# Kernel optimization log

Hardware: AMD Instinct MI355X
Metric: run time of the kernel (lower is better)

## Reference

```python
import jax, jax.numpy as jnp
import numpy as np

B, C, H, W = 8, 64, 56, 56
PLANES = 64
EPS = 1e-5


def conv2d(x, w, b, stride=1, pad=1):
    out = jax.lax.conv_general_dilated(
        x, w, window_strides=(stride, stride), padding=[(pad, pad), (pad, pad)],
        dimension_numbers=('NCHW', 'OIHW', 'NCHW'))
    return out + b[None, :, None, None]


def _bilinear_gather(img, py, px):
    # img: [C,H,W]; py/px: [K2,Ho,Wo] float sample coords; zero outside bounds
    Ci, Hi, Wi = img.shape
    y0 = jnp.floor(py); x0 = jnp.floor(px)
    wy1 = py - y0; wx1 = px - x0
    wy0 = 1.0 - wy1; wx0 = 1.0 - wx1

    def g(yc, xc):
        valid = ((yc >= 0) & (yc < Hi) & (xc >= 0) & (xc < Wi)).astype(img.dtype)
        yi = jnp.clip(yc, 0, Hi - 1).astype(jnp.int32)
        xi = jnp.clip(xc, 0, Wi - 1).astype(jnp.int32)
        return img[:, yi, xi] * valid[None]  # [C,K2,Ho,Wo]

    return (g(y0, x0) * (wy0 * wx0)[None] + g(y0, x0 + 1) * (wy0 * wx1)[None]
            + g(y0 + 1, x0) * (wy1 * wx0)[None] + g(y0 + 1, x0 + 1) * (wy1 * wx1)[None])


def deform_conv2d(x, offset, weight, stride, pad, dil):
    # torchvision DeformConv2d semantics (no mask). offset: [B, 2*K2, Ho, Wo]
    Bx, Cx, Hx, Wx = x.shape
    O, _, kh, kw = weight.shape
    K2 = kh * kw
    Ho, Wo = offset.shape[2], offset.shape[3]
    off = offset.reshape(Bx, K2, 2, Ho, Wo)
    dy, dx = off[:, :, 0], off[:, :, 1]
    ki, kj = jnp.meshgrid(jnp.arange(kh), jnp.arange(kw), indexing='ij')
    base_y = (ki.reshape(-1) * dil - pad).astype(x.dtype)  # [K2]
    base_x = (kj.reshape(-1) * dil - pad).astype(x.dtype)
    hg = (jnp.arange(Ho) * stride).astype(x.dtype)
    wg = (jnp.arange(Wo) * stride).astype(x.dtype)
    py = dy + base_y[None, :, None, None] + hg[None, None, :, None]
    px = dx + base_x[None, :, None, None] + wg[None, None, None, :]
    cols = jax.vmap(_bilinear_gather)(x, py, px)  # [B,C,K2,Ho,Wo]
    return jnp.einsum('bckhw,ock->bohw', cols, weight.reshape(O, Cx, K2))


def bn(x, gamma, beta, mean, var):
    inv = gamma / jnp.sqrt(var + EPS)
    return x * inv[None, :, None, None] + (beta - mean * inv)[None, :, None, None]


def setup_inputs() -> dict:
    key = jax.random.key(0)
    ks = jax.random.split(key, 12)
    s = 0.05
    d = {
        'x':   jax.random.normal(ks[0], (B, C, H, W), jnp.float32),
        'ow1': jax.random.normal(ks[1], (2 * 9, C, 3, 3), jnp.float32) * s,
        'ob1': jnp.zeros((2 * 9,), jnp.float32),
        'ow3': jax.random.normal(ks[2], (2 * 25, C, 3, 3), jnp.float32) * s,
        'ob3': jnp.zeros((2 * 25,), jnp.float32),
        'ow2': jax.random.normal(ks[3], (2 * 9, PLANES, 3, 3), jnp.float32) * s,
        'ob2': jnp.zeros((2 * 9,), jnp.float32),
        'w1':  jax.random.normal(ks[4], (PLANES, C, 3, 3), jnp.float32) * s,
        'w3':  jax.random.normal(ks[5], (PLANES, C, 5, 5), jnp.float32) * s,
        'w2':  jax.random.normal(ks[6], (PLANES, PLANES, 3, 3), jnp.float32) * s,
    }
    for i, tag in zip((7, 8, 9), ('1', '3', '2')):
        d['g' + tag] = jnp.ones((PLANES,), jnp.float32)
        d['b' + tag] = jnp.zeros((PLANES,), jnp.float32)
        d['m' + tag] = jax.random.normal(ks[i], (PLANES,), jnp.float32) * 0.1
        d['v' + tag] = jnp.ones((PLANES,), jnp.float32)
    return d


def reference(x, ow1, ob1, ow3, ob3, ow2, ob2, w1, w3, w2,
              g1, b1, m1, v1, g3, b3, m3, v3, g2, b2, m2, v2):
    offset1 = conv2d(x, ow1, ob1, stride=1, pad=1)
    out = jax.nn.relu(bn(deform_conv2d(x, offset1, w1, 1, 2, 2), g1, b1, m1, v1))
    offset3 = conv2d(x, ow3, ob3, stride=1, pad=1)
    out_1 = jax.nn.relu(bn(deform_conv2d(x, offset3, w3, 1, 4, 2), g3, b3, m3, v3))
    out = out + out_1
    offset2 = conv2d(out, ow2, ob2, stride=1, pad=1)
    out = bn(deform_conv2d(out, offset2, w2, 1, 2, 2), g2, b2, m2, v2)
    out = out + x  # identity shortcut (stride=1, in_planes==planes)
    return jax.nn.relu(out)
```

## Files before the change

kernel.cpp:

```cpp
#include <hip/hip_runtime.h>
#include <math.h>

#define HD 56
#define WD 56
#define CD 64
#define PLANE 3136

typedef _Float16 f16x8 __attribute__((ext_vector_type(8)));
typedef _Float16 f16x4 __attribute__((ext_vector_type(4)));
typedef _Float16 f16x2 __attribute__((ext_vector_type(2)));
typedef float    f32x4 __attribute__((ext_vector_type(4)));

__global__ __launch_bounds__(256) void wtrans_k(
    const float* __restrict__ w1, const float* __restrict__ w3, const float* __restrict__ w2,
    const float* __restrict__ ow1, const float* __restrict__ ow3, const float* __restrict__ ow2,
    _Float16* __restrict__ t1, _Float16* __restrict__ t3, _Float16* __restrict__ t2,
    _Float16* __restrict__ owF, _Float16* __restrict__ owT2)
{
    int y = blockIdx.y;
    if (y == 0 || y == 1 || y == 2) {
        const float* src = (y == 0) ? w1 : (y == 1) ? w3 : w2;
        _Float16* dst    = (y == 0) ? t1 : (y == 1) ? t3 : t2;
        int K2 = (y == 1) ? 25 : 9;
        int total = 64 * 64 * K2;
        for (int idx = blockIdx.x * 256 + threadIdx.x; idx < total; idx += gridDim.x * 256) {
            int k = idx >> 12;
            int o = (idx >> 6) & 63;
            int c = idx & 63;
            dst[idx] = (_Float16)src[(o * 64 + c) * K2 + k];
        }
    } else if (y == 3) {
        int total = 9 * 32 * 64;
        for (int idx = blockIdx.x * 256 + threadIdx.x; idx < total; idx += gridDim.x * 256) {
            int k = idx >> 11;
            int o = (idx >> 6) & 31;
            int c = idx & 63;
            owF[k * 6144 + o * 64 + c] = (o < 18) ? (_Float16)ow1[(o * 64 + c) * 9 + k] : (_Float16)0.f;
        }
    } else if (y == 4) {
        int total = 9 * 64 * 64;
        for (int idx = blockIdx.x * 256 + threadIdx.x; idx < total; idx += gridDim.x * 256) {
            int k = idx >> 12;
            int o = (idx >> 6) & 63;
            int c = idx & 63;
            owF[k * 6144 + (32 + o) * 64 + c] = (o < 50) ? (_Float16)ow3[(o * 64 + c) * 9 + k] : (_Float16)0.f;
        }
    } else {
        int total = 9 * 32 * 64;
        for (int idx = blockIdx.x * 256 + threadIdx.x; idx < total; idx += gridDim.x * 256) {
            int k = idx >> 11;
            int o = (idx >> 6) & 31;
            int c = idx & 63;
            owT2[k * 2048 + o * 64 + c] = (o < 18) ? (_Float16)ow2[(o * 64 + c) * 9 + k] : (_Float16)0.f;
        }
    }
}

__global__ __launch_bounds__(256) void xt_k(const float* __restrict__ src, _Float16* __restrict__ dst)
{
    int b  = blockIdx.y;
    int px = blockIdx.x * 64 + (threadIdx.x & 63);
    int cg = threadIdx.x >> 6;
    const float* s = src + (size_t)b * CD * PLANE + px;
    f16x8 lo, hi;
#pragma unroll
    for (int i = 0; i < 8; ++i) lo[i] = (_Float16)s[(cg * 16 + i) * PLANE];
#pragma unroll
    for (int i = 0; i < 8; ++i) hi[i] = (_Float16)s[(cg * 16 + 8 + i) * PLANE];
    _Float16* d = dst + ((size_t)b * PLANE + px) * 64 + cg * 16;
    *(f16x8*)d = lo;
    *(f16x8*)(d + 8) = hi;
}

template<int NTILES, int OP>
__device__ inline void af_load(const _Float16* __restrict__ ow, int k, int off, f16x8* s) {
    const _Float16* wk = ow + k * (OP * 64);
#pragma unroll
    for (int t = 0; t < NTILES; ++t) s[t] = *(const f16x8*)(wk + (t * 16) * 64 + off);
}

template<int FUSED>
__global__ __launch_bounds__(256) void offc_k(
    const _Float16* __restrict__ src,
    const _Float16* __restrict__ ow,
    const float* __restrict__ biasA, const float* __restrict__ biasB,
    uint4* __restrict__ tbl)
{
    constexpr int NTILES = FUSED ? 6 : 2;
    constexpr int OP     = FUSED ? 96 : 32;
    constexpr int NTT    = FUSED ? 34 : 9;
    __shared__ float red[4][NTILES * 4 * 64];

    int tid = threadIdx.x;
    int bid = blockIdx.x;
    int b    = bid & 7;
    int tile = bid >> 3;
    int l = tid & 63;
    int n = l & 15;
    int g = l >> 4;
    int w = tid >> 6;
    int tg = w >> 1;
    int pix = tile * 16 + n;
    int ho = pix / WD, wo = pix - ho * WD;
    int ckoff = (w & 1) * 32 + g * 8;
    int afo = n * 64 + ckoff;
    const _Float16* sp = src + ((size_t)b * PLANE + pix) * 64 + ckoff;

    f32x4 acc[NTILES];
#pragma unroll
    for (int t = 0; t < NTILES; ++t) acc[t] = (f32x4){0.f, 0.f, 0.f, 0.f};

#define NB(K, D) { int ky_=(K)/3-1, kx_=(K)%3-1; int yn_=ho+ky_, xn_=wo+kx_;       \
    f16x8 z_ = {(_Float16)0,(_Float16)0,(_Float16)0,(_Float16)0,                   \
                (_Float16)0,(_Float16)0,(_Float16)0,(_Float16)0};                  \
    D = z_;                                                                        \
    if ((unsigned)yn_ < (unsigned)HD && (unsigned)xn_ < (unsigned)WD)              \
        D = *(const f16x8*)(sp + (ky_ * WD + kx_) * 64); }

#define MFMAS(S, NBV) { _Pragma("unroll")                                          \
    for (int t = 0; t < NTILES; ++t)                                               \
        acc[t] = __builtin_amdgcn_mfma_f32_16x16x32_f16((S)[t], NBV, acc[t], 0, 0, 0); }

    f16x8 sA[NTILES], sB[NTILES];
    if (tg == 0) {
        f16x8 nb0, nb1, nb2, nb3, nb4;
        NB(0, nb0) NB(1, nb1) NB(2, nb2) NB(3, nb3) NB(4, nb4)
        af_load<NTILES, OP>(ow, 0, afo, sA);
        af_load<NTILES, OP>(ow, 1, afo, sB); MFMAS(sA, nb0)
        af_load<NTILES, OP>(ow, 2, afo, sA); MFMAS(sB, nb1)
        af_load<NTILES, OP>(ow, 3, afo, sB); MFMAS(sA, nb2)
        af_load<NTILES, OP>(ow, 4, afo, sA); MFMAS(sB, nb3)
        MFMAS(sA, nb4)
    } else {
        f16x8 nb0, nb1, nb2, nb3;
        NB(5, nb0) NB(6, nb1) NB(7, nb2) NB(8, nb3)
        af_load<NTILES, OP>(ow, 5, afo, sA);
        af_load<NTILES, OP>(ow, 6, afo, sB); MFMAS(sA, nb0)
        af_load<NTILES, OP>(ow, 7, afo, sA); MFMAS(sB, nb1)
        af_load<NTILES, OP>(ow, 8, afo, sB); MFMAS(sA, nb2)
        MFMAS(sB, nb3)
    }
#undef NB
#undef MFMAS

#pragma unroll
    for (int t = 0; t < NTILES; ++t)
#pragma unroll
        for (int rr = 0; rr < 4; ++rr)
            red[w][(t * 4 + rr) * 64 + l] = acc[t][rr];
    __syncthreads();

#pragma unroll
    for (int tt = 0; tt < (NTILES + 3) / 4; ++tt) {
        int t = w + tt * 4;
        if (t < NTILES) {
            float v[4];
#pragma unroll
            for (int rr = 0; rr < 4; ++rr) {
                int ia = (t * 4 + rr) * 64 + l;
                v[rr] = red[0][ia] + red[1][ia] + red[2][ia] + red[3][ia];
            }
            int obase = t * 16 + g * 4;
            bool isB = FUSED && (t >= 2);
            int oc0 = isB ? (obase - 32) : obase;
            const float* bp = isB ? biasB : biasA;
#pragma unroll
            for (int pp = 0; pp < 2; ++pp) {
                int oce = oc0 + pp * 2;
                int kl  = oce >> 1;
                int kmax = isB ? 25 : 9;
                if (kl < kmax) {
                    float dy = v[pp * 2]     + bp[oce];
                    float dx = v[pp * 2 + 1] + bp[oce + 1];
                    int by, bx;
                    if (isB) { int q = kl / 5; by = q * 2 - 4; bx = (kl - q * 5) * 2 - 4; }
                    else     { int q = kl / 3; by = q * 2 - 2; bx = (kl - q * 3) * 2 - 2; }
                    float py = dy + (float)(by + ho);
                    float px = dx + (float)(bx + wo);
                    float fy = floorf(py), fx = floorf(px);
                    float wy1 = py - fy, wx1 = px - fx;
                    float wy0 = 1.f - wy1, wx0 = 1.f - wx1;
                    int y0 = (int)fy, x0 = (int)fx;
                    int y1 = y0 + 1, x1 = x0 + 1;
                    float vy0 = (y0 >= 0 && y0 < HD) ? 1.f : 0.f;
                    float vy1 = (y1 >= 0 && y1 < HD) ? 1.f : 0.f;
                    float vx0 = (x0 >= 0 && x0 < WD) ? 1.f : 0.f;
                    float vx1 = (x1 >= 0 && x1 < WD) ? 1.f : 0.f;
                    int cy0 = min(max(y0, 0), HD - 1), cy1 = min(max(y1, 0), HD - 1);
                    int cx0 = min(max(x0, 0), WD - 1), cx1 = min(max(x1, 0), WD - 1);
                    unsigned i00 = (unsigned)(cy0 * WD + cx0), i01 = (unsigned)(cy0 * WD + cx1);
                    unsigned i10 = (unsigned)(cy1 * WD + cx0), i11 = (unsigned)(cy1 * WD + cx1);
                    f16x2 wl = {(_Float16)(wy0 * wx0 * vy0 * vx0), (_Float16)(wy0 * wx1 * vy0 * vx1)};
                    f16x2 wh = {(_Float16)(wy1 * wx0 * vy1 * vx0), (_Float16)(wy1 * wx1 * vy1 * vx1)};
                    uint4 e;
                    e.x = i00 | (i01 << 16);
                    e.y = i10 | (i11 << 16);
                    e.z = __builtin_bit_cast(unsigned int, wl);
                    e.w = __builtin_bit_cast(unsigned int, wh);
                    int gtap = isB ? (9 + kl) : kl;
                    tbl[((size_t)(b * NTT + gtap)) * PLANE + pix] = e;
                }
            }
        }
    }
}

template<int MERGED>
__global__ __launch_bounds__(MERGED ? 512 : 256) void dconv_k(
    const _Float16* __restrict__ xt,
    const uint4* __restrict__ tbl,
    const _Float16* __restrict__ wTA, const _Float16* __restrict__ wTB,
    const float* __restrict__ gA, const float* __restrict__ bA,
    const float* __restrict__ mA, const float* __restrict__ vA,
    const float* __restrict__ gB, const float* __restrict__ bB,
    const float* __restrict__ mB, const float* __restrict__ vB,
    const float* __restrict__ addsrc, float* __restrict__ out,
    _Float16* __restrict__ outh)
{
    constexpr int NT = MERGED ? 34 : 9;
    constexpr int NW = MERGED ? 8 : 4;
    __shared__ float red[NW - 1][16 * 64];

    int tid = threadIdx.x;
    int bid = blockIdx.x;
    int b    = bid & 7;
    int tile = bid >> 3;
    int l   = tid & 63;
    int n   = l & 15;
    int g   = l >> 4;
    int w   = tid >> 6;
    int kh  = w & 1;
    int tg  = w >> 1;
    int pix = tile * 16 + n;
    int ckoff = kh * 32 + g * 8;

    int base, cnt;
    if (MERGED) { base = (tg == 0) ? 0 : (tg == 1) ? 9 : (tg == 2) ? 18 : 26; cnt = (tg < 2) ? 9 : 8; }
    else        { base = tg ? 5 : 0; cnt = tg ? 4 : 5; }
    int lastT = base + cnt - 1;

    const _Float16* xp = xt + (size_t)b * PLANE * 64 + ckoff;
    const uint4*    tp = tbl + (size_t)b * NT * PLANE + pix;
    int afoff = n * 64 + ckoff;

    f32x4 acc[4];
#pragma unroll
    for (int ot = 0; ot < 4; ++ot) acc[ot] = (f32x4){0.f, 0.f, 0.f, 0.f};

#define DECL_STG(S) f16x8 S##c0, S##c1, S##c2, S##c3, S##a0, S##a1, S##a2, S##a3; \
                    unsigned S##wz, S##ww
    DECL_STG(s0);
    DECL_STG(s1);
#undef DECL_STG

#define ISSUE(S, E, T) {                                                      \
    unsigned i00_ = (E).x & 0xffffu, i01_ = (E).x >> 16;                      \
    unsigned i10_ = (E).y & 0xffffu, i11_ = (E).y >> 16;                      \
    S##wz = (E).z; S##ww = (E).w;                                             \
    S##c0 = *(const f16x8*)(xp + i00_ * 64);                                  \
    S##c1 = *(const f16x8*)(xp + i01_ * 64);                                  \
    S##c2 = *(const f16x8*)(xp + i10_ * 64);                                  \
    S##c3 = *(const f16x8*)(xp + i11_ * 64);                                  \
    const _Float16* wk_ = (!MERGED || (T) < 9) ? (wTA + (T) * 4096)           \
                                               : (wTB + ((T) - 9) * 4096);    \
    S##a0 = *(const f16x8*)(wk_ + afoff);                                     \
    S##a1 = *(const f16x8*)(wk_ + afoff + 1024);                              \
    S##a2 = *(const f16x8*)(wk_ + afoff + 2048);                              \
    S##a3 = *(const f16x8*)(wk_ + afoff + 3072); }

#define CONSUME(S) {                                                          \
    f16x2 wl_ = __builtin_bit_cast(f16x2, S##wz);                             \
    f16x2 wh_ = __builtin_bit_cast(f16x2, S##ww);                             \
    f16x8 bf_ = S##c0 * wl_.x + S##c1 * wl_.y + S##c2 * wh_.x + S##c3 * wh_.y;\
    acc[0] = __builtin_amdgcn_mfma_f32_16x16x32_f16(S##a0, bf_, acc[0], 0, 0, 0); \
    acc[1] = __builtin_amdgcn_mfma_f32_16x16x32_f16(S##a1, bf_, acc[1], 0, 0, 0); \
    acc[2] = __builtin_amdgcn_mfma_f32_16x16x32_f16(S##a2, bf_, acc[2], 0, 0, 0); \
    acc[3] = __builtin_amdgcn_mfma_f32_16x16x32_f16(S##a3, bf_, acc[3], 0, 0, 0); }

    {
        uint4 e0 = tp[base * PLANE];
        uint4 e1 = tp[(base + 1) * PLANE];
        ISSUE(s0, e0, base)
        ISSUE(s1, e1, base + 1)
    }
    uint4 E0 = tp[min(base + 2, lastT) * PLANE];
    uint4 E1 = tp[min(base + 3, lastT) * PLANE];

    int j = 0;
#pragma unroll 1
    for (; j + 1 < cnt; j += 2) {
        CONSUME(s0)
        if (j + 2 < cnt) {
            ISSUE(s0, E0, base + j + 2)
            E0 = tp[min(base + j + 4, lastT) * PLANE];
        }
        CONSUME(s1)
        if (j + 3 < cnt) {
            ISSUE(s1, E1, base + j + 3)
            E1 = tp[min(base + j + 5, lastT) * PLANE];
        }
    }
    if (j < cnt) CONSUME(s0)
#undef ISSUE
#undef CONSUME

    if (w > 0) {
#pragma unroll
        for (int ot = 0; ot < 4; ++ot)
#pragma unroll
            for (int rr = 0; rr < 4; ++rr)
                red[w - 1][(ot * 4 + rr) * 64 + l] = acc[ot][rr];
    }
    __syncthreads();
    if (w == 0) {
#pragma unroll
        for (int ot = 0; ot < 4; ++ot) {
            float r[4];
#pragma unroll
            for (int rr = 0; rr < 4; ++rr) {
                int ia = (ot * 4 + rr) * 64 + l;
                int o = ot * 16 + g * 4 + rr;
                if (MERGED) {
                    float sumA = acc[ot][rr] + red[0][ia];
                    float sumB = red[1][ia] + red[2][ia] + red[3][ia]
                               + red[4][ia] + red[5][ia] + red[6][ia];
                    float ivA = gA[o] * (1.f / sqrtf(vA[o] + 1e-5f));
                    float shA = bA[o] - mA[o] * ivA;
                    float ivB = gB[o] * (1.f / sqrtf(vB[o] + 1e-5f));
                    float shB = bB[o] - mB[o] * ivB;
                    r[rr] = fmaxf(sumA * ivA + shA, 0.f) + fmaxf(sumB * ivB + shB, 0.f);
                } else {
                    float s = acc[ot][rr] + red[0][ia] + red[1][ia] + red[2][ia];
                    float iv = gA[o] * (1.f / sqrtf(vA[o] + 1e-5f));
                    float sh = bA[o] - mA[o] * iv;
                    size_t oidx = (size_t)(b * 64 + o) * PLANE + pix;
                    out[oidx] = fmaxf(s * iv + sh + addsrc[oidx], 0.f);
                }
            }
            if (MERGED) {
                f16x4 hv = {(_Float16)r[0], (_Float16)r[1], (_Float16)r[2], (_Float16)r[3]};
                *(f16x4*)(outh + ((size_t)b * PLANE + pix) * 64 + ot * 16 + g * 4) = hv;
            }
        }
    }
}

extern "C" void kernel_launch(void* const* d_in, const int* in_sizes, int n_in,
                              void* d_out, int out_size, void* d_ws, size_t ws_size,
                              hipStream_t stream) {
    const float* x   = (const float*)d_in[0];
    const float* ow1 = (const float*)d_in[1];
    const float* ob1 = (const float*)d_in[2];
    const float* ow3 = (const float*)d_in[3];
    const float* ob3 = (const float*)d_in[4];
    const float* ow2 = (const float*)d_in[5];
    const float* ob2 = (const float*)d_in[6];
    const float* w1  = (const float*)d_in[7];
    const float* w3  = (const float*)d_in[8];
    const float* w2  = (const float*)d_in[9];
    const float* g1  = (const float*)d_in[10];
    const float* b1  = (const float*)d_in[11];
    const float* m1  = (const float*)d_in[12];
    const float* v1  = (const float*)d_in[13];
    const float* g3  = (const float*)d_in[14];
    const float* b3  = (const float*)d_in[15];
    const float* m3  = (const float*)d_in[16];
    const float* v3  = (const float*)d_in[17];
    const float* g2  = (const float*)d_in[18];
    const float* b2  = (const float*)d_in[19];
    const float* m2  = (const float*)d_in[20];
    const float* v2  = (const float*)d_in[21];

    float* out = (float*)d_out;
    float* ws  = (float*)d_ws;

    _Float16* xth  = (_Float16*)ws;
    _Float16* mth  = (_Float16*)(ws + 802816);
    uint4*    tbl  = (uint4*)(ws + 1605632);
    _Float16* wT1h = (_Float16*)(ws + 5017600);
    _Float16* wT3h = wT1h + 36864;
    _Float16* wT2h = wT3h + 102400;
    _Float16* owFh = wT2h + 36864;
    _Float16* owT2h= owFh + 55296;

    wtrans_k<<<dim3(16, 6), dim3(256), 0, stream>>>(
        w1, w3, w2, ow1, ow3, ow2, wT1h, wT3h, wT2h, owFh, owT2h);
    xt_k<<<dim3(49, 8), dim3(256), 0, stream>>>(x, xth);

    offc_k<1><<<dim3(1568), dim3(256), 0, stream>>>(xth, owFh, ob1, ob3, tbl);

    dconv_k<1><<<dim3(1568), dim3(512), 0, stream>>>(
        xth, tbl, wT1h, wT3h, g1, b1, m1, v1, g3, b3, m3, v3, nullptr, nullptr, mth);

    offc_k<0><<<dim3(1568), dim3(256), 0, stream>>>(mth, owT2h, ob2, ob2, tbl);

    dconv_k<0><<<dim3(1568), dim3(256), 0, stream>>>(
        mth, tbl, wT2h, wT2h, g2, b2, m2, v2, g2, b2, m2, v2, x, out, nullptr);
}
```

Before: 201.7 us.

## Split deformable conv into separate bilinear gather and MFMA GEMM kernels

The fused gather-plus-MFMA deformable conv kernel is replaced by two kernels. A gather kernel materialises the bilinearly interpolated columns into a workspace buffer laid out in channel groups of 8 halfs. A GEMM kernel then reads those columns with 32-pixel tiles and splits taps across 4 warps. This aims to stop random gathers from stalling the MFMA pipeline, at the cost of an extra write and read of a large column buffer (up to about 27 MB) and possible batch chunking when the workspace is small.

```diff
diff --git a/kernel.cpp b/kernel.cpp
--- a/kernel.cpp
+++ b/kernel.cpp
@@ -5,6 +5,7 @@
 #define WD 56
 #define CD 64
 #define PLANE 3136
+#define CPL (PLANE * 8)
 
 typedef _Float16 f16x8 __attribute__((ext_vector_type(8)));
 typedef _Float16 f16x4 __attribute__((ext_vector_type(4)));
@@ -205,141 +206,136 @@
     }
 }
 
+__global__ __launch_bounds__(256) void gather_k(
+    const _Float16* __restrict__ src,
+    const uint4* __restrict__ tbl,
+    _Float16* __restrict__ cols, int NT, int b0)
+{
+    int pix = blockIdx.x * 256 + threadIdx.x;
+    if (pix >= PLANE) return;
+    int tap = blockIdx.y;
+    int bg  = blockIdx.z;
+    int b   = b0 + bg;
+    uint4 e = tbl[((size_t)(b * NT + tap)) * PLANE + pix];
+    unsigned i00 = e.x & 0xffffu, i01 = e.x >> 16;
+    unsigned i10 = e.y & 0xffffu, i11 = e.y >> 16;
+    f16x2 wl = __builtin_bit_cast(f16x2, e.z);
+    f16x2 wh = __builtin_bit_cast(f16x2, e.w);
+    const _Float16* xp = src + (size_t)b * PLANE * 64;
+    const f16x8* p00 = (const f16x8*)(xp + i00 * 64);
+    const f16x8* p01 = (const f16x8*)(xp + i01 * 64);
+    const f16x8* p10 = (const f16x8*)(xp + i10 * 64);
+    const f16x8* p11 = (const f16x8*)(xp + i11 * 64);
+    _Float16* cb = cols + (size_t)(bg * NT + tap) * 8 * CPL + pix * 8;
+#pragma unroll
+    for (int j = 0; j < 8; ++j) {
+        f16x8 v = p00[j] * wl.x + p01[j] * wl.y + p10[j] * wh.x + p11[j] * wh.y;
+        *(f16x8*)(cb + (size_t)j * CPL) = v;
+    }
+}
+
 template<int MERGED>
-__global__ __launch_bounds__(MERGED ? 512 : 256) void dconv_k(
-    const _Float16* __restrict__ xt,
-    const uint4* __restrict__ tbl,
+__global__ __launch_bounds__(256) void gemm_k(
+    const _Float16* __restrict__ cols,
     const _Float16* __restrict__ wTA, const _Float16* __restrict__ wTB,
     const float* __restrict__ gA, const float* __restrict__ bA,
     const float* __restrict__ mA, const float* __restrict__ vA,
     const float* __restrict__ gB, const float* __restrict__ bB,
     const float* __restrict__ mB, const float* __restrict__ vB,
     const float* __restrict__ addsrc, float* __restrict__ out,
-    _Float16* __restrict__ outh)
+    _Float16* __restrict__ outh, int b0, int Gm, int Gs)
 {
     constexpr int NT = MERGED ? 34 : 9;
-    constexpr int NW = MERGED ? 8 : 4;
-    __shared__ float red[NW - 1][16 * 64];
+    __shared__ float red[3][2][16 * 64];
 
     int tid = threadIdx.x;
     int bid = blockIdx.x;
-    int b    = bid & 7;
-    int tile = bid >> 3;
-    int l   = tid & 63;
-    int n   = l & 15;
-    int g   = l >> 4;
-    int w   = tid >> 6;
-    int kh  = w & 1;
-    int tg  = w >> 1;
-    int pix = tile * 16 + n;
-    int ckoff = kh * 32 + g * 8;
+    int bg   = bid & Gm;
+    int tp   = bid >> Gs;
+    int b    = b0 + bg;
+    int l = tid & 63;
+    int n = l & 15;
+    int g = l >> 4;
+    int w = tid >> 6;
 
     int base, cnt;
-    if (MERGED) { base = (tg == 0) ? 0 : (tg == 1) ? 9 : (tg == 2) ? 18 : 26; cnt = (tg < 2) ? 9 : 8; }
-    else        { base = tg ? 5 : 0; cnt = tg ? 4 : 5; }
-    int lastT = base + cnt - 1;
-
-    const _Float16* xp = xt + (size_t)b * PLANE * 64 + ckoff;
-    const uint4*    tp = tbl + (size_t)b * NT * PLANE + pix;
-    int afoff = n * 64 + ckoff;
-
-    f32x4 acc[4];
-#pragma unroll
-    for (int ot = 0; ot < 4; ++ot) acc[ot] = (f32x4){0.f, 0.f, 0.f, 0.f};
-
-#define DECL_STG(S) f16x8 S##c0, S##c1, S##c2, S##c3, S##a0, S##a1, S##a2, S##a3; \
-                    unsigned S##wz, S##ww
-    DECL_STG(s0);
-    DECL_STG(s1);
-#undef DECL_STG
-
-#define ISSUE(S, E, T) {                                                      \
-    unsigned i00_ = (E).x & 0xffffu, i01_ = (E).x >> 16;                      \
-    unsigned i10_ = (E).y & 0xffffu, i11_ = (E).y >> 16;                      \
-    S##wz = (E).z; S##ww = (E).w;                                             \
-    S##c0 = *(const f16x8*)(xp + i00_ * 64);                                  \
-    S##c1 = *(const f16x8*)(xp + i01_ * 64);                                  \
-    S##c2 = *(const f16x8*)(xp + i10_ * 64);                                  \
-    S##c3 = *(const f16x8*)(xp + i11_ * 64);                                  \
-    const _Float16* wk_ = (!MERGED || (T) < 9) ? (wTA + (T) * 4096)           \
-                                               : (wTB + ((T) - 9) * 4096);    \
-    S##a0 = *(const f16x8*)(wk_ + afoff);                                     \
-    S##a1 = *(const f16x8*)(wk_ + afoff + 1024);                              \
-    S##a2 = *(const f16x8*)(wk_ + afoff + 2048);                              \
-    S##a3 = *(const f16x8*)(wk_ + afoff + 3072); }
-
-#define CONSUME(S) {                                                          \
-    f16x2 wl_ = __builtin_bit_cast(f16x2, S##wz);                             \
-    f16x2 wh_ = __builtin_bit_cast(f16x2, S##ww);                             \
-    f16x8 bf_ = S##c0 * wl_.x + S##c1 * wl_.y + S##c2 * wh_.x + S##c3 * wh_.y;\
-    acc[0] = __builtin_amdgcn_mfma_f32_16x16x32_f16(S##a0, bf_, acc[0], 0, 0, 0); \
-    acc[1] = __builtin_amdgcn_mfma_f32_16x16x32_f16(S##a1, bf_, acc[1], 0, 0, 0); \
-    acc[2] = __builtin_amdgcn_mfma_f32_16x16x32_f16(S##a2, bf_, acc[2], 0, 0, 0); \
-    acc[3] = __builtin_amdgcn_mfma_f32_16x16x32_f16(S##a3, bf_, acc[3], 0, 0, 0); }
-
-    {
-        uint4 e0 = tp[base * PLANE];
-        uint4 e1 = tp[(base + 1) * PLANE];
-        ISSUE(s0, e0, base)
-        ISSUE(s1, e1, base + 1)
-    }
-    uint4 E0 = tp[min(base + 2, lastT) * PLANE];
-    uint4 E1 = tp[min(base + 3, lastT) * PLANE];
-
-    int j = 0;
-#pragma unroll 1
-    for (; j + 1 < cnt; j += 2) {
-        CONSUME(s0)
-        if (j + 2 < cnt) {
-            ISSUE(s0, E0, base + j + 2)
-            E0 = tp[min(base + j + 4, lastT) * PLANE];
-        }
-        CONSUME(s1)
-        if (j + 3 < cnt) {
-            ISSUE(s1, E1, base + j + 3)
-            E1 = tp[min(base + j + 5, lastT) * PLANE];
-        }
-    }
-    if (j < cnt) CONSUME(s0)
-#undef ISSUE
-#undef CONSUME
+    if (MERGED) { base = (w == 0) ? 0 : (w == 1) ? 9 : (w == 2) ? 17 : 25;
+                  cnt  = (w == 0) ? 9 : (w == 3) ? 9 : 8; }
+    else        { base = (w == 0) ? 0 : (w == 1) ? 3 : (w == 2) ? 5 : 7;
+                  cnt  = (w == 0) ? 3 : 2; }
+
+    int afoff = n * 64 + g * 8;
+    int px0   = tp * 32 + n;
+    const _Float16* cbase = cols + (size_t)bg * NT * 8 * CPL;
+
+    f32x4 acc[2][4];
+#pragma unroll
+    for (int st = 0; st < 2; ++st)
+#pragma unroll
+        for (int ot = 0; ot < 4; ++ot) acc[st][ot] = (f32x4){0.f, 0.f, 0.f, 0.f};
+
+#pragma unroll 2
+    for (int j = 0; j < cnt; ++j) {
+        int t = base + j;
+        const _Float16* wk = (!MERGED || t < 9) ? (wTA + t * 4096) : (wTB + (t - 9) * 4096);
+        const _Float16* cp_lo = cbase + (size_t)(t * 8 + g) * CPL + px0 * 8;
+        const _Float16* cp_hi = cbase + (size_t)(t * 8 + 4 + g) * CPL + px0 * 8;
+        f16x8 b0lo = *(const f16x8*)cp_lo;
+        f16x8 b0hi = *(const f16x8*)cp_hi;
+        f16x8 b1lo = *(const f16x8*)(cp_lo + 128);
+        f16x8 b1hi = *(const f16x8*)(cp_hi + 128);
+#pragma unroll
+        for (int ot = 0; ot < 4; ++ot) {
+            f16x8 aflo = *(const f16x8*)(wk + afoff + ot * 1024);
+            f16x8 afhi = *(const f16x8*)(wk + afoff + ot * 1024 + 32);
+            acc[0][ot] = __builtin_amdgcn_mfma_f32_16x16x32_f16(aflo, b0lo, acc[0][ot], 0, 0, 0);
+            acc[0][ot] = __builtin_amdgcn_mfma_f32_16x16x32_f16(afhi, b0hi, acc[0][ot], 0, 0, 0);
+            acc[1][ot] = __builtin_amdgcn_mfma_f32_16x16x32_f16(aflo, b1lo, acc[1][ot], 0, 0, 0);
+            acc[1][ot] = __builtin_amdgcn_mfma_f32_16x16x32_f16(afhi, b1hi, acc[1][ot], 0, 0, 0);
+        }
+    }
 
     if (w > 0) {
 #pragma unroll
-        for (int ot = 0; ot < 4; ++ot)
-#pragma unroll
-            for (int rr = 0; rr < 4; ++rr)
-                red[w - 1][(ot * 4 + rr) * 64 + l] = acc[ot][rr];
+        for (int st = 0; st < 2; ++st)
+#pragma unroll
+            for (int ot = 0; ot < 4; ++ot)
+#pragma unroll
+                for (int rr = 0; rr < 4; ++rr)
+                    red[w - 1][st][(ot * 4 + rr) * 64 + l] = acc[st][ot][rr];
     }
     __syncthreads();
     if (w == 0) {
 #pragma unroll
-        for (int ot = 0; ot < 4; ++ot) {
-            float r[4];
-#pragma unroll
-            for (int rr = 0; rr < 4; ++rr) {
-                int ia = (ot * 4 + rr) * 64 + l;
-                int o = ot * 16 + g * 4 + rr;
+        for (int st = 0; st < 2; ++st) {
+            int pix = px0 + st * 16;
+#pragma unroll
+            for (int ot = 0; ot < 4; ++ot) {
+                float r[4];
+#pragma unroll
+                for (int rr = 0; rr < 4; ++rr) {
+                    int ia = (ot * 4 + rr) * 64 + l;
+                    int o = ot * 16 + g * 4 + rr;
+                    if (MERGED) {
+                        float sumA = acc[st][ot][rr];
+                        float sumB = red[0][st][ia] + red[1][st][ia] + red[2][st][ia];
+                        float ivA = gA[o] * (1.f / sqrtf(vA[o] + 1e-5f));
+                        float shA = bA[o] - mA[o] * ivA;
+                        float ivB = gB[o] * (1.f / sqrtf(vB[o] + 1e-5f));
+                        float shB = bB[o] - mB[o] * ivB;
+                        r[rr] = fmaxf(sumA * ivA + shA, 0.f) + fmaxf(sumB * ivB + shB, 0.f);
+                    } else {
+                        float s = acc[st][ot][rr] + red[0][st][ia] + red[1][st][ia] + red[2][st][ia];
+                        float iv = gA[o] * (1.f / sqrtf(vA[o] + 1e-5f));
+                        float sh = bA[o] - mA[o] * iv;
+                        size_t oidx = (size_t)(b * 64 + o) * PLANE + pix;
+                        out[oidx] = fmaxf(s * iv + sh + addsrc[oidx], 0.f);
+                    }
+                }
                 if (MERGED) {
-                    float sumA = acc[ot][rr] + red[0][ia];
-                    float sumB = red[1][ia] + red[2][ia] + red[3][ia]
-                               + red[4][ia] + red[5][ia] + red[6][ia];
-                    float ivA = gA[o] * (1.f / sqrtf(vA[o] + 1e-5f));
-                    float shA = bA[o] - mA[o] * ivA;
-                    float ivB = gB[o] * (1.f / sqrtf(vB[o] + 1e-5f));
-                    float shB = bB[o] - mB[o] * ivB;
-                    r[rr] = fmaxf(sumA * ivA + shA, 0.f) + fmaxf(sumB * ivB + shB, 0.f);
-                } else {
-                    float s = acc[ot][rr] + red[0][ia] + red[1][ia] + red[2][ia];
-                    float iv = gA[o] * (1.f / sqrtf(vA[o] + 1e-5f));
-                    float sh = bA[o] - mA[o] * iv;
-                    size_t oidx = (size_t)(b * 64 + o) * PLANE + pix;
-                    out[oidx] = fmaxf(s * iv + sh + addsrc[oidx], 0.f);
+                    f16x4 hv = {(_Float16)r[0], (_Float16)r[1], (_Float16)r[2], (_Float16)r[3]};
+                    *(f16x4*)(outh + ((size_t)b * PLANE + pix) * 64 + ot * 16 + g * 4) = hv;
                 }
-            }
-            if (MERGED) {
-                f16x4 hv = {(_Float16)r[0], (_Float16)r[1], (_Float16)r[2], (_Float16)r[3]};
-                *(f16x4*)(outh + ((size_t)b * PLANE + pix) * 64 + ot * 16 + g * 4) = hv;
             }
         }
     }
@@ -372,16 +368,26 @@
     const float* v2  = (const float*)d_in[21];
 
     float* out = (float*)d_out;
-    float* ws  = (float*)d_ws;
-
-    _Float16* xth  = (_Float16*)ws;
-    _Float16* mth  = (_Float16*)(ws + 802816);
-    uint4*    tbl  = (uint4*)(ws + 1605632);
-    _Float16* wT1h = (_Float16*)(ws + 5017600);
+    char*  wsb = (char*)d_ws;
+
+    _Float16* xth  = (_Float16*)wsb;
+    _Float16* mth  = xth + 1605632;
+    _Float16* wT1h = mth + 1605632;
     _Float16* wT3h = wT1h + 36864;
     _Float16* wT2h = wT3h + 102400;
     _Float16* owFh = wT2h + 36864;
     _Float16* owT2h= owFh + 55296;
+    uint4*    tbl  = (uint4*)(wsb + 6922240);
+    _Float16* colsh= (_Float16*)(wsb + 20570112);
+    size_t fixedB = 20570112;
+
+    int G = 8;
+    while (G > 1 && fixedB + (size_t)G * 34 * 3136 * 128 > ws_size) G >>= 1;
+    int Gs = (G == 8) ? 3 : (G == 4) ? 2 : (G == 2) ? 1 : 0;
+    size_t colsCapPlanes = (size_t)G * 34;
+    int G2 = 8;
+    while (G2 > 1 && (size_t)G2 * 9 > colsCapPlanes) G2 >>= 1;
+    int G2s = (G2 == 8) ? 3 : (G2 == 4) ? 2 : (G2 == 2) ? 1 : 0;
 
     wtrans_k<<<dim3(16, 6), dim3(256), 0, stream>>>(
         w1, w3, w2, ow1, ow3, ow2, wT1h, wT3h, wT2h, owFh, owT2h);
@@ -389,11 +395,19 @@
 
     offc_k<1><<<dim3(1568), dim3(256), 0, stream>>>(xth, owFh, ob1, ob3, tbl);
 
-    dconv_k<1><<<dim3(1568), dim3(512), 0, stream>>>(
-        xth, tbl, wT1h, wT3h, g1, b1, m1, v1, g3, b3, m3, v3, nullptr, nullptr, mth);
+    for (int b0 = 0; b0 < 8; b0 += G) {
+        gather_k<<<dim3(13, 34, G), dim3(256), 0, stream>>>(xth, tbl, colsh, 34, b0);
+        gemm_k<1><<<dim3(98 * G), dim3(256), 0, stream>>>(
+            colsh, wT1h, wT3h, g1, b1, m1, v1, g3, b3, m3, v3,
+            nullptr, nullptr, mth, b0, G - 1, Gs);
+    }
 
     offc_k<0><<<dim3(1568), dim3(256), 0, stream>>>(mth, owT2h, ob2, ob2, tbl);
 
-    dconv_k<0><<<dim3(1568), dim3(256), 0, stream>>>(
-        mth, tbl, wT2h, wT2h, g2, b2, m2, v2, g2, b2, m2, v2, x, out, nullptr);
-}
+    for (int b0 = 0; b0 < 8; b0 += G2) {
+        gather_k<<<dim3(13, 9, G2), dim3(256), 0, stream>>>(mth, tbl, colsh, 9, b0);
+        gemm_k<0><<<dim3(98 * G2), dim3(256), 0, stream>>>(
+            colsh, wT2h, wT2h, g2, b2, m2, v2, g2, b2, m2, v2,
+            x, out, nullptr, b0, G2 - 1, G2s);
+    }
+}
```

After: 236.1 us. 17.0% more time.
